# Kernel optimization log

Hardware: AMD Instinct MI355X
Metric: run time of the kernel (lower is better)

The kernel has to match this reference:

```python
import jax, jax.numpy as jnp
import numpy as np

B, T, D, H = 8, 1024, 512, 8
HD = D // H  # per-head hidden = embed_dim // n_head = 64
EPS = 1e-5


def setup_inputs() -> dict:
    key = jax.random.key(0)
    ks = jax.random.split(key, 8)
    x = jax.random.normal(ks[0], (B, T, D), dtype=jnp.float32)
    sc = 1.0 / np.sqrt(D)
    Wq = jax.random.normal(ks[1], (D, H * HD), dtype=jnp.float32) * sc
    Wk = jax.random.normal(ks[2], (D, H * HD), dtype=jnp.float32) * sc
    Wp = jax.random.normal(ks[3], (H * HD, D), dtype=jnp.float32) * sc
    bq = jnp.zeros((H * HD,), jnp.float32)
    bk = jnp.zeros((H * HD,), jnp.float32)
    bp = jnp.zeros((D,), jnp.float32)
    w_mlp = jax.random.normal(ks[4], (2 * HD,), dtype=jnp.float32) * 0.1
    ln_g = jnp.ones((D,), jnp.float32)
    ln_b = jnp.zeros((D,), jnp.float32)
    return {"x": x, "Wq": Wq, "bq": bq, "Wk": Wk, "bk": bk,
            "Wp": Wp, "bp": bp, "w_mlp": w_mlp, "ln_g": ln_g, "ln_b": ln_b}


def reference(x, Wq, bq, Wk, bk, Wp, bp, w_mlp, ln_g, ln_b):
    b, t, d = x.shape
    h, hd = H, HD
    # q/k projections, split into heads: [B,T,H,hd]
    qx = (x @ Wq + bq).reshape(b, t, h, hd)
    kx = (x @ Wk + bk).reshape(b, t, h, hd)
    # MLP score: tanh(concat(k_j, q_i) . w) == tanh(k_j.w[:hd] + q_i.w[hd:])
    k_s = jnp.einsum('bkhd,d->bkh', kx, w_mlp[:hd])   # [B,K,H]
    q_s = jnp.einsum('bqhd,d->bqh', qx, w_mlp[hd:])   # [B,Q,H]
    score = jnp.tanh(q_s[:, :, None, :] + k_s[:, None, :, :])  # [B,Q,K,H]
    attn = jax.nn.softmax(score, axis=2)  # softmax over k_len
    # values are the key projection kx (bmm(score, kx) in original)
    out = jnp.einsum('bqkh,bkhd->bqhd', attn, kx).reshape(b, t, h * hd)
    out = out @ Wp + bp  # output projection (dropout is identity at eval)
    # residual + LayerNorm
    y = x + out
    mu = jnp.mean(y, axis=-1, keepdims=True)
    var = jnp.var(y, axis=-1, keepdims=True)
    yn = (y - mu) * jax.lax.rsqrt(var + EPS)
    return yn * ln_g + ln_b
```

## Files before the change

### kernel.cpp

```cpp
#include <hip/hip_runtime.h>
#include <cstddef>

#define TT 1024
#define DDIM 512
#define HH 8
#define NND 128
#define NS 68

typedef __attribute__((ext_vector_type(8))) short bfrag;
typedef __attribute__((ext_vector_type(4))) float facc;

#define SC2   2.8853900817779268f
#define L2E   1.4426950408889634f

static __device__ __forceinline__ unsigned bfrne(float f) {
    unsigned u = __float_as_uint(f);
    return (u + 0x7fffu + ((u >> 16) & 1u)) >> 16;
}
static __device__ __forceinline__ unsigned pack2rne(float a, float b) {
    return bfrne(a) | (bfrne(b) << 16);
}
static __device__ __forceinline__ unsigned pack2hu(float a, float b) {
    return ((__float_as_uint(a) + 0x8000u) >> 16) |
           ((__float_as_uint(b) + 0x8000u) & 0xffff0000u);
}
static __device__ __forceinline__ void gl2lds16(const void* g, void* l) {
    __builtin_amdgcn_global_load_lds(
        (const __attribute__((address_space(1))) unsigned int*)g,
        (__attribute__((address_space(3))) unsigned int*)l, 16, 0, 0);
}
static __device__ __forceinline__ float wfun(float z2) {
    float t = __builtin_amdgcn_exp2f(z2);
    float r = __builtin_amdgcn_rcpf(t + 1.f);
    return __builtin_amdgcn_exp2f(fmaf(r, -2.f * L2E, L2E));
}

__global__ __launch_bounds__(256) void prepare_kernel(
    const float* __restrict__ x, const float* __restrict__ Wk,
    const float* __restrict__ Wp, const float* __restrict__ Wq,
    const float* __restrict__ bq, const float* __restrict__ wm,
    unsigned short* __restrict__ xb, unsigned short* __restrict__ WkT,
    unsigned short* __restrict__ WpT, unsigned short* __restrict__ vq2b,
    float* __restrict__ qsb2)
{
    const int bx = blockIdx.x, tid = threadIdx.x;
    if (bx < 2048) {
        const int lane = tid & 63, wave = tid >> 6;
        const int row = bx * 4 + wave;
        const float4* xr = (const float4*)(x + (size_t)row * DDIM);
        float4 x0 = xr[lane * 2], x1 = xr[lane * 2 + 1];
        uint4 st;
        st.x = pack2rne(x0.x, x0.y); st.y = pack2rne(x0.z, x0.w);
        st.z = pack2rne(x1.x, x1.y); st.w = pack2rne(x1.z, x1.w);
        int p = lane ^ (row & 7);
        *(uint4*)(xb + (size_t)row * DDIM + p * 8) = st;
    } else if (bx < 2176) {
        int idx = bx - 2048;
        const float* src = (idx & 64) ? Wp : Wk;
        unsigned short* dst = (idx & 64) ? WpT : WkT;
        idx &= 63;
        const int n0 = (idx & 7) * 64, k0 = (idx >> 3) * 64;
        __shared__ float sT[64][65];
        #pragma unroll
        for (int it = 0; it < 4; ++it) {
            int task = it * 256 + tid;
            int kr = task >> 4, c4 = (task & 15) * 4;
            float4 v = *(const float4*)(src + (size_t)(k0 + kr) * DDIM + n0 + c4);
            sT[kr][c4] = v.x; sT[kr][c4 + 1] = v.y; sT[kr][c4 + 2] = v.z; sT[kr][c4 + 3] = v.w;
        }
        __syncthreads();
        #pragma unroll
        for (int it = 0; it < 2; ++it) {
            int task = it * 256 + tid;
            int n = task >> 3, kg = task & 7;
            unsigned u[4];
            #pragma unroll
            for (int jj = 0; jj < 4; ++jj)
                u[jj] = pack2rne(sT[kg * 8 + jj * 2][n], sT[kg * 8 + jj * 2 + 1][n]);
            int p = ((k0 >> 3) + kg) ^ (n & 7);
            uint4 st; st.x = u[0]; st.y = u[1]; st.z = u[2]; st.w = u[3];
            *(uint4*)(dst + (size_t)(n0 + n) * DDIM + p * 8) = st;
        }
    } else {
        int idx = (bx - 2176) * 256 + tid;
        int h = idx >> 9, d = idx & 511;
        float s = 0.f;
        #pragma unroll 8
        for (int j = 0; j < 64; ++j)
            s = fmaf(Wq[(size_t)d * DDIM + h * 64 + j], wm[64 + j], s);
        vq2b[h * DDIM + d] = (unsigned short)bfrne(s * SC2);
        if (idx < HH) {
            float sb = 0.f;
            for (int j = 0; j < 64; ++j)
                sb = fmaf(bq[idx * 64 + j], wm[64 + j], sb);
            qsb2[idx] = sb * SC2;
        }
    }
}

__global__ __launch_bounds__(256) void gemm1_kernel(
    const unsigned short* __restrict__ A, const unsigned short* __restrict__ B,
    const float* __restrict__ bias, unsigned short* __restrict__ kxTg,
    float* __restrict__ ks2, const float* __restrict__ wm,
    const unsigned short* __restrict__ vq2b, const float* __restrict__ qsb2,
    float* __restrict__ qs2)
{
    __shared__ __align__(16) unsigned short smem[12288];
    unsigned short* sA = smem;
    unsigned short* sB = smem + 8192;
    const int tid = threadIdx.x, lane = tid & 63, wave = tid >> 6;
    const int l15 = lane & 15, quad = lane >> 4;
    const int h = blockIdx.x, row0 = blockIdx.y * 128;
    const int col0 = h * 64;

    facc acc[2][4]; facc accq[2];
    #pragma unroll
    for (int i = 0; i < 2; ++i) {
        #pragma unroll
        for (int j = 0; j < 4; ++j) { acc[i][j][0]=0.f; acc[i][j][1]=0.f; acc[i][j][2]=0.f; acc[i][j][3]=0.f; }
        accq[i][0]=0.f; accq[i][1]=0.f; accq[i][2]=0.f; accq[i][3]=0.f;
    }

    for (int k0 = 0; k0 < 512; k0 += 64) {
        #pragma unroll
        for (int it = 0; it < 4; ++it) {
            int g = it * 256 + tid;
            int r = g >> 3, kg = g & 7;
            gl2lds16(A + (size_t)(row0 + r) * 512 + k0 + kg * 8, &sA[g * 8]);
        }
        #pragma unroll
        for (int it = 0; it < 2; ++it) {
            int g = it * 256 + tid;
            int r = g >> 3, kg = g & 7;
            gl2lds16(B + (size_t)(col0 + r) * 512 + k0 + kg * 8, &sB[g * 8]);
        }
        __syncthreads();
        #pragma unroll
        for (int ks_ = 0; ks_ < 2; ++ks_) {
            int slot = (ks_ * 4 + quad) ^ (l15 & 7);
            bfrag a[2], b[4];
            #pragma unroll
            for (int i = 0; i < 2; ++i)
                a[i] = *(const bfrag*)&sA[(wave * 32 + i * 16 + l15) * 64 + slot * 8];
            #pragma unroll
            for (int nt = 0; nt < 4; ++nt)
                b[nt] = *(const bfrag*)&sB[(nt * 16 + l15) * 64 + slot * 8];
            bfrag bvq = *(const bfrag*)(vq2b + h * 512 + k0 + ks_ * 32 + quad * 8);
            #pragma unroll
            for (int i = 0; i < 2; ++i) {
                #pragma unroll
                for (int nt = 0; nt < 4; ++nt)
                    acc[i][nt] = __builtin_amdgcn_mfma_f32_16x16x32_bf16(a[i], b[nt], acc[i][nt], 0, 0, 0);
                accq[i] = __builtin_amdgcn_mfma_f32_16x16x32_bf16(a[i], bvq, accq[i], 0, 0, 0);
            }
        }
        __syncthreads();
    }

    const int bb = row0 >> 10, t0 = row0 & 1023;
    const float qsbh = qsb2[h];
    float bvv[4], wmv[4];
    #pragma unroll
    for (int nt = 0; nt < 4; ++nt) {
        bvv[nt] = bias[col0 + nt * 16 + l15];
        wmv[nt] = wm[nt * 16 + l15] * SC2;
    }
    float part[2][4];
    #pragma unroll
    for (int i = 0; i < 2; ++i)
        #pragma unroll
        for (int r = 0; r < 4; ++r) part[i][r] = 0.f;

    unsigned short* eT = smem;
    #pragma unroll
    for (int i = 0; i < 2; ++i) {
        int tr = wave * 32 + i * 16 + quad * 4;
        #pragma unroll
        for (int nt = 0; nt < 4; ++nt) {
            int col = nt * 16 + l15;
            float v0 = acc[i][nt][0] + bvv[nt], v1 = acc[i][nt][1] + bvv[nt];
            float v2 = acc[i][nt][2] + bvv[nt], v3 = acc[i][nt][3] + bvv[nt];
            part[i][0] = fmaf(wmv[nt], v0, part[i][0]);
            part[i][1] = fmaf(wmv[nt], v1, part[i][1]);
            part[i][2] = fmaf(wmv[nt], v2, part[i][2]);
            part[i][3] = fmaf(wmv[nt], v3, part[i][3]);
            *(unsigned*)&eT[col * 136 + tr]     = pack2rne(v0, v1);
            *(unsigned*)&eT[col * 136 + tr + 2] = pack2rne(v2, v3);
        }
    }
    #pragma unroll
    for (int i = 0; i < 2; ++i)
        #pragma unroll
        for (int r = 0; r < 4; ++r) {
            float p = part[i][r];
            p += __shfl_xor(p, 1); p += __shfl_xor(p, 2);
            p += __shfl_xor(p, 4); p += __shfl_xor(p, 8);
            if (l15 == 0) {
                size_t o = (size_t)(bb * HH + h) * TT + t0 + wave * 32 + i * 16 + quad * 4 + r;
                ks2[o] = p;
                qs2[o] = accq[i][r] + qsbh;
            }
        }
    __syncthreads();
    unsigned short* kxbase = kxTg + ((size_t)(bb * HH + h) * 64) * TT;
    #pragma unroll
    for (int it = 0; it < 4; ++it) {
        int task = it * 256 + tid;
        int col = task >> 4, seg = task & 15;
        uint4 v = *(const uint4*)&eT[col * 136 + seg * 8];
        int g = (t0 >> 3) + seg;
        int p = g ^ (col & 7);
        *(uint4*)(kxbase + (size_t)col * TT + p * 8) = v;
    }
}

__global__ __launch_bounds__(256) void attn_kernel(
    const unsigned short* __restrict__ kxTg, const float* __restrict__ qs2,
    const float* __restrict__ ks2, unsigned short* __restrict__ attb)
{
    __shared__ __align__(16) unsigned short kxT[64 * 256];
    __shared__ float ksc[1024];
    __shared__ float redl[8];
    __shared__ __align__(16) float nodes[NND * NS];
    const int bh = blockIdx.x >> 1, thalf = blockIdx.x & 1;
    const int b = bh >> 3, h = bh & 7;
    const int tid = threadIdx.x, lane = tid & 63, wave = tid >> 6;
    const int l15 = lane & 15, quad = lane >> 4;

    ((float4*)ksc)[tid] = ((const float4*)(ks2 + (size_t)bh * TT))[tid];
    float4 q4 = ((const float4*)(qs2 + (size_t)bh * TT))[tid];
    float mn = fminf(fminf(q4.x, q4.y), fminf(q4.z, q4.w));
    float mx = fmaxf(fmaxf(q4.x, q4.y), fmaxf(q4.z, q4.w));
    #pragma unroll
    for (int off = 32; off > 0; off >>= 1) {
        mn = fminf(mn, __shfl_xor(mn, off));
        mx = fmaxf(mx, __shfl_xor(mx, off));
    }
    if (lane == 0) { redl[wave] = mn; redl[4 + wave] = mx; }
    __syncthreads();
    const float mnv = fminf(fminf(redl[0], redl[1]), fminf(redl[2], redl[3]));
    const float mxv = fmaxf(fmaxf(redl[4], redl[5]), fmaxf(redl[6], redl[7]));
    const float h2v = (mxv - mnv) * (1.f / 127.f);
    const float inv127v = 127.f / fmaxf(mxv - mnv, 1e-12f);
    const float zA = mnv + (wave * 16 + l15) * h2v;
    const float zB = zA + 64.f * h2v;

    const unsigned short* kxbase = kxTg + (size_t)bh * 64 * TT;
    facc acc[2][4]; facc accZ[2];
    #pragma unroll
    for (int g = 0; g < 2; ++g) {
        #pragma unroll
        for (int i = 0; i < 4; ++i) { acc[g][i][0]=0.f; acc[g][i][1]=0.f; acc[g][i][2]=0.f; acc[g][i][3]=0.f; }
        accZ[g][0]=0.f; accZ[g][1]=0.f; accZ[g][2]=0.f; accZ[g][3]=0.f;
    }
    bfrag ones;
    #pragma unroll
    for (int j = 0; j < 8; ++j) ones[j] = (short)0x3F80;

    for (int ck = 0; ck < 4; ++ck) {
        #pragma unroll
        for (int it = 0; it < 8; ++it) {
            int g = it * 256 + tid;
            int d = g >> 5, j = g & 31;
            gl2lds16(kxbase + (size_t)d * TT + ck * 256 + j * 8, &kxT[g * 8]);
        }
        __syncthreads();
        #pragma unroll
        for (int kst = 0; kst < 8; ++kst) {
            const float* kvp = &ksc[ck * 256 + kst * 32 + quad * 8];
            float4 kv0 = *(const float4*)kvp;
            float4 kv1 = *(const float4*)(kvp + 4);
            int slot = (kst * 4 + quad) ^ (l15 & 7);
            bfrag bf_[4];
            #pragma unroll
            for (int dt = 0; dt < 4; ++dt)
                bf_[dt] = *(const bfrag*)&kxT[(dt * 16 + l15) * 256 + slot * 8];
            #pragma unroll
            for (int g = 0; g < 2; ++g) {
                float z = g ? zB : zA;
                union { unsigned u[4]; bfrag f; } afu;
                afu.u[0] = pack2hu(wfun(z + kv0.x), wfun(z + kv0.y));
                afu.u[1] = pack2hu(wfun(z + kv0.z), wfun(z + kv0.w));
                afu.u[2] = pack2hu(wfun(z + kv1.x), wfun(z + kv1.y));
                afu.u[3] = pack2hu(wfun(z + kv1.z), wfun(z + kv1.w));
                #pragma unroll
                for (int dt = 0; dt < 4; ++dt)
                    acc[g][dt] = __builtin_amdgcn_mfma_f32_16x16x32_bf16(afu.f, bf_[dt], acc[g][dt], 0, 0, 0);
                accZ[g] = __builtin_amdgcn_mfma_f32_16x16x32_bf16(afu.f, ones, accZ[g], 0, 0, 0);
            }
        }
        __syncthreads();
    }
    #pragma unroll
    for (int g = 0; g < 2; ++g) {
        #pragma unroll
        for (int r = 0; r < 4; ++r) {
            int node = g * 64 + wave * 16 + quad * 4 + r;
            #pragma unroll
            for (int dt = 0; dt < 4; ++dt)
                nodes[node * NS + dt * 16 + l15] = acc[g][dt][r];
            if (l15 == 0) nodes[node * NS + 64] = accZ[g][r];
        }
    }
    __syncthreads();

    const float* qsp = qs2 + (size_t)bh * TT;
    #pragma unroll 2
    for (int it = 0; it < 32; ++it) {
        int task = it * 256 + tid;
        int t = thalf * 512 + (task >> 4), dp = task & 15;
        float qv = qsp[t];
        float u = (qv - mnv) * inv127v;
        int i = (int)floorf(u) - 1;
        i = i < 0 ? 0 : (i > NND - 4 ? NND - 4 : i);
        float s = u - (float)i;
        float s1 = s - 1.f, s2 = s - 2.f, s3 = s - 3.f;
        float w0 = -s1 * s2 * s3 * (1.f / 6.f);
        float w1 = s * s2 * s3 * 0.5f;
        float w2 = -s * s1 * s3 * 0.5f;
        float w3 = s * s1 * s2 * (1.f / 6.f);
        const float* base = &nodes[i * NS];
        float4 v0 = *(const float4*)(base + 4 * dp);
        float4 v1 = *(const float4*)(base + NS + 4 * dp);
        float4 v2 = *(const float4*)(base + 2 * NS + 4 * dp);
        float4 v3 = *(const float4*)(base + 3 * NS + 4 * dp);
        float zz = w0 * base[64] + w1 * base[NS + 64] + w2 * base[2 * NS + 64] + w3 * base[3 * NS + 64];
        float ox = w0 * v0.x + w1 * v1.x + w2 * v2.x + w3 * v3.x;
        float oy = w0 * v0.y + w1 * v1.y + w2 * v2.y + w3 * v3.y;
        float oz = w0 * v0.z + w1 * v1.z + w2 * v2.z + w3 * v3.z;
        float ow = w0 * v0.w + w1 * v1.w + w2 * v2.w + w3 * v3.w;
        float rz = __builtin_amdgcn_rcpf(zz);
        uint2 st;
        st.x = pack2rne(ox * rz, oy * rz);
        st.y = pack2rne(oz * rz, ow * rz);
        int row = b * TT + t;
        int col = h * 64 + 4 * dp;
        int p = (col >> 3) ^ (row & 7);
        *(uint2*)&attb[(size_t)row * DDIM + p * 8 + (col & 7)] = st;
    }
}

__global__ __launch_bounds__(256) void gemm2_kernel(
    const unsigned short* __restrict__ A, const unsigned short* __restrict__ B,
    const float* __restrict__ bias, const float* __restrict__ x,
    unsigned short* __restrict__ yb)
{
    __shared__ __align__(16) unsigned short smem[12288];
    unsigned short* sA = smem;
    unsigned short* sB = smem + 8192;
    const int tid = threadIdx.x, lane = tid & 63, wave = tid >> 6;
    const int l15 = lane & 15, quad = lane >> 4;
    const int col0 = blockIdx.x * 64, row0 = blockIdx.y * 128;

    facc acc[2][4];
    #pragma unroll
    for (int i = 0; i < 2; ++i)
        #pragma unroll
        for (int j = 0; j < 4; ++j) { acc[i][j][0]=0.f; acc[i][j][1]=0.f; acc[i][j][2]=0.f; acc[i][j][3]=0.f; }

    for (int k0 = 0; k0 < 512; k0 += 64) {
        #pragma unroll
        for (int it = 0; it < 4; ++it) {
            int g = it * 256 + tid;
            int r = g >> 3, kg = g & 7;
            gl2lds16(A + (size_t)(row0 + r) * 512 + k0 + kg * 8, &sA[g * 8]);
        }
        #pragma unroll
        for (int it = 0; it < 2; ++it) {
            int g = it * 256 + tid;
            int r = g >> 3, kg = g & 7;
            gl2lds16(B + (size_t)(col0 + r) * 512 + k0 + kg * 8, &sB[g * 8]);
        }
        __syncthreads();
        #pragma unroll
        for (int ks_ = 0; ks_ < 2; ++ks_) {
            int slot = (ks_ * 4 + quad) ^ (l15 & 7);
            bfrag a[2], b[4];
            #pragma unroll
            for (int i = 0; i < 2; ++i)
                a[i] = *(const bfrag*)&sA[(wave * 32 + i * 16 + l15) * 64 + slot * 8];
            #pragma unroll
            for (int nt = 0; nt < 4; ++nt)
                b[nt] = *(const bfrag*)&sB[(nt * 16 + l15) * 64 + slot * 8];
            #pragma unroll
            for (int i = 0; i < 2; ++i)
                #pragma unroll
                for (int nt = 0; nt < 4; ++nt)
                    acc[i][nt] = __builtin_amdgcn_mfma_f32_16x16x32_bf16(a[i], b[nt], acc[i][nt], 0, 0, 0);
        }
        __syncthreads();
    }
    float bvv[4];
    #pragma unroll
    for (int nt = 0; nt < 4; ++nt) bvv[nt] = bias[col0 + nt * 16 + l15];
    unsigned short* yT = smem;
    #pragma unroll
    for (int i = 0; i < 2; ++i) {
        #pragma unroll
        for (int nt = 0; nt < 4; ++nt) {
            int col = nt * 16 + l15;
            #pragma unroll
            for (int r = 0; r < 4; ++r) {
                int row = wave * 32 + i * 16 + quad * 4 + r;
                float xv = x[(size_t)(row0 + row) * DDIM + col0 + col];
                float y = acc[i][nt][r] + bvv[nt] + xv;
                yT[row * 72 + col] = (unsigned short)bfrne(y);
            }
        }
    }
    __syncthreads();
    #pragma unroll
    for (int it = 0; it < 4; ++it) {
        int task = it * 256 + tid;
        int row = task >> 3, seg = task & 7;
        uint4 v = *(const uint4*)&yT[row * 72 + seg * 8];
        *(uint4*)(yb + (size_t)(row0 + row) * DDIM + col0 + seg * 8) = v;
    }
}

__global__ __launch_bounds__(256) void ln_kernel(
    const unsigned short* __restrict__ yb, const float* __restrict__ g,
    const float* __restrict__ bet, float* __restrict__ out)
{
    const int tid = threadIdx.x, lane = tid & 63, wave = tid >> 6;
    const int row = blockIdx.x * 4 + wave;
    uint4 v = *(const uint4*)(yb + (size_t)row * DDIM + lane * 8);
    float y[8];
    y[0] = __uint_as_float(v.x << 16); y[1] = __uint_as_float(v.x & 0xffff0000u);
    y[2] = __uint_as_float(v.y << 16); y[3] = __uint_as_float(v.y & 0xffff0000u);
    y[4] = __uint_as_float(v.z << 16); y[5] = __uint_as_float(v.z & 0xffff0000u);
    y[6] = __uint_as_float(v.w << 16); y[7] = __uint_as_float(v.w & 0xffff0000u);
    float s = 0.f, s2 = 0.f;
    #pragma unroll
    for (int i = 0; i < 8; ++i) { s += y[i]; s2 = fmaf(y[i], y[i], s2); }
    #pragma unroll
    for (int off = 32; off > 0; off >>= 1) {
        s += __shfl_xor(s, off);
        s2 += __shfl_xor(s2, off);
    }
    float mu = s * (1.f / 512.f);
    float var = s2 * (1.f / 512.f) - mu * mu;
    float inv = rsqrtf(var + 1e-5f);
    const float4* gp = (const float4*)(g + lane * 8);
    const float4* bp = (const float4*)(bet + lane * 8);
    float4 g0 = gp[0], g1 = gp[1], b0 = bp[0], b1 = bp[1];
    float4 o0, o1;
    o0.x = (y[0] - mu) * inv * g0.x + b0.x; o0.y = (y[1] - mu) * inv * g0.y + b0.y;
    o0.z = (y[2] - mu) * inv * g0.z + b0.z; o0.w = (y[3] - mu) * inv * g0.w + b0.w;
    o1.x = (y[4] - mu) * inv * g1.x + b1.x; o1.y = (y[5] - mu) * inv * g1.y + b1.y;
    o1.z = (y[6] - mu) * inv * g1.z + b1.z; o1.w = (y[7] - mu) * inv * g1.w + b1.w;
    float4* op = (float4*)(out + (size_t)row * DDIM);
    op[lane * 2] = o0; op[lane * 2 + 1] = o1;
}

extern "C" void kernel_launch(void* const* d_in, const int* in_sizes, int n_in,
                              void* d_out, int out_size, void* d_ws, size_t ws_size,
                              hipStream_t stream)
{
    const float* x    = (const float*)d_in[0];
    const float* Wq   = (const float*)d_in[1];
    const float* bq   = (const float*)d_in[2];
    const float* Wk   = (const float*)d_in[3];
    const float* bk   = (const float*)d_in[4];
    const float* Wp   = (const float*)d_in[5];
    const float* bp   = (const float*)d_in[6];
    const float* wm   = (const float*)d_in[7];
    const float* ln_g = (const float*)d_in[8];
    const float* ln_b = (const float*)d_in[9];
    float* out = (float*)d_out;

    float* ws = (float*)d_ws;
    float*          qsb2 = ws;
    unsigned short* vq2b = (unsigned short*)(ws + 64);
    unsigned short* WkT  = (unsigned short*)(ws + 2112);
    unsigned short* WpT  = (unsigned short*)(ws + 133184);
    unsigned short* xb   = (unsigned short*)(ws + 264256);
    unsigned short* kxTg = (unsigned short*)(ws + 2361408);
    float*          qs2  = ws + 4458560;
    float*          ks2  = ws + 4524096;
    unsigned short* attb = (unsigned short*)(ws + 4589632);
    unsigned short* yb   = xb;

    prepare_kernel<<<2192, 256, 0, stream>>>(x, Wk, Wp, Wq, bq, wm,
                                             xb, WkT, WpT, vq2b, qsb2);
    gemm1_kernel<<<dim3(8, 64), 256, 0, stream>>>(xb, WkT, bk, kxTg, ks2, wm,
                                                  vq2b, qsb2, qs2);
    attn_kernel<<<128, 256, 0, stream>>>(kxTg, qs2, ks2, attb);
    gemm2_kernel<<<dim3(8, 64), 256, 0, stream>>>(attb, WpT, bp, x, yb);
    ln_kernel<<<2048, 256, 0, stream>>>(yb, ln_g, ln_b, out);
}
```

Measured before the change: 153.1 us.

## Widen GEMM tiles to 128x128 and move residual add into LayerNorm

Both projection GEMMs now use 128x128 output tiles computed by a 2x2 wave grid, replacing 128x64 tiles. Each block covers two heads in gemm1 and twice the columns in gemm2, which raises operand reuse per LDS load but halves the block count to 256. The residual add moves out of the gemm2 epilogue into the LayerNorm kernel, which reads the already-swizzled bf16 copy of x rather than fp32 x. This trades residual precision for less traffic, and needs a separate yb buffer. The attention grid is also remapped to a 2D launch.

```diff
diff --git a/kernel.cpp b/kernel.cpp
--- a/kernel.cpp
+++ b/kernel.cpp
@@ -105,17 +105,18 @@
     const unsigned short* __restrict__ vq2b, const float* __restrict__ qsb2,
     float* __restrict__ qs2)
 {
-    __shared__ __align__(16) unsigned short smem[12288];
+    __shared__ __align__(16) unsigned short smem[17408];
     unsigned short* sA = smem;
     unsigned short* sB = smem + 8192;
     const int tid = threadIdx.x, lane = tid & 63, wave = tid >> 6;
     const int l15 = lane & 15, quad = lane >> 4;
-    const int h = blockIdx.x, row0 = blockIdx.y * 128;
-    const int col0 = h * 64;
-
-    facc acc[2][4]; facc accq[2];
-    #pragma unroll
-    for (int i = 0; i < 2; ++i) {
+    const int wr = wave >> 1, wc = wave & 1;
+    const int row0 = blockIdx.x * 128, colpair = blockIdx.y;
+    const int h = colpair * 2 + wc, n0 = colpair * 128;
+
+    facc acc[4][4]; facc accq[4];
+    #pragma unroll
+    for (int i = 0; i < 4; ++i) {
         #pragma unroll
         for (int j = 0; j < 4; ++j) { acc[i][j][0]=0.f; acc[i][j][1]=0.f; acc[i][j][2]=0.f; acc[i][j][3]=0.f; }
         accq[i][0]=0.f; accq[i][1]=0.f; accq[i][2]=0.f; accq[i][3]=0.f;
@@ -127,27 +128,21 @@
             int g = it * 256 + tid;
             int r = g >> 3, kg = g & 7;
             gl2lds16(A + (size_t)(row0 + r) * 512 + k0 + kg * 8, &sA[g * 8]);
-        }
-        #pragma unroll
-        for (int it = 0; it < 2; ++it) {
-            int g = it * 256 + tid;
-            int r = g >> 3, kg = g & 7;
-            gl2lds16(B + (size_t)(col0 + r) * 512 + k0 + kg * 8, &sB[g * 8]);
+            gl2lds16(B + (size_t)(n0 + r) * 512 + k0 + kg * 8, &sB[g * 8]);
         }
         __syncthreads();
         #pragma unroll
         for (int ks_ = 0; ks_ < 2; ++ks_) {
             int slot = (ks_ * 4 + quad) ^ (l15 & 7);
-            bfrag a[2], b[4];
-            #pragma unroll
-            for (int i = 0; i < 2; ++i)
-                a[i] = *(const bfrag*)&sA[(wave * 32 + i * 16 + l15) * 64 + slot * 8];
-            #pragma unroll
-            for (int nt = 0; nt < 4; ++nt)
-                b[nt] = *(const bfrag*)&sB[(nt * 16 + l15) * 64 + slot * 8];
+            bfrag a[4], b[4];
+            #pragma unroll
+            for (int i = 0; i < 4; ++i) {
+                a[i] = *(const bfrag*)&sA[(wr * 64 + i * 16 + l15) * 64 + slot * 8];
+                b[i] = *(const bfrag*)&sB[(wc * 64 + i * 16 + l15) * 64 + slot * 8];
+            }
             bfrag bvq = *(const bfrag*)(vq2b + h * 512 + k0 + ks_ * 32 + quad * 8);
             #pragma unroll
-            for (int i = 0; i < 2; ++i) {
+            for (int i = 0; i < 4; ++i) {
                 #pragma unroll
                 for (int nt = 0; nt < 4; ++nt)
                     acc[i][nt] = __builtin_amdgcn_mfma_f32_16x16x32_bf16(a[i], b[nt], acc[i][nt], 0, 0, 0);
@@ -162,55 +157,56 @@
     float bvv[4], wmv[4];
     #pragma unroll
     for (int nt = 0; nt < 4; ++nt) {
-        bvv[nt] = bias[col0 + nt * 16 + l15];
+        bvv[nt] = bias[h * 64 + nt * 16 + l15];
         wmv[nt] = wm[nt * 16 + l15] * SC2;
     }
-    float part[2][4];
-    #pragma unroll
-    for (int i = 0; i < 2; ++i)
+    float part[4][4];
+    #pragma unroll
+    for (int i = 0; i < 4; ++i)
         #pragma unroll
         for (int r = 0; r < 4; ++r) part[i][r] = 0.f;
 
-    unsigned short* eT = smem;
-    #pragma unroll
-    for (int i = 0; i < 2; ++i) {
-        int tr = wave * 32 + i * 16 + quad * 4;
+    unsigned short* eT = smem + wc * 8704;
+    #pragma unroll
+    for (int i = 0; i < 4; ++i) {
+        int tr = wr * 64 + i * 16 + quad * 4;
         #pragma unroll
         for (int nt = 0; nt < 4; ++nt) {
-            int col = nt * 16 + l15;
+            int d = nt * 16 + l15;
             float v0 = acc[i][nt][0] + bvv[nt], v1 = acc[i][nt][1] + bvv[nt];
             float v2 = acc[i][nt][2] + bvv[nt], v3 = acc[i][nt][3] + bvv[nt];
             part[i][0] = fmaf(wmv[nt], v0, part[i][0]);
             part[i][1] = fmaf(wmv[nt], v1, part[i][1]);
             part[i][2] = fmaf(wmv[nt], v2, part[i][2]);
             part[i][3] = fmaf(wmv[nt], v3, part[i][3]);
-            *(unsigned*)&eT[col * 136 + tr]     = pack2rne(v0, v1);
-            *(unsigned*)&eT[col * 136 + tr + 2] = pack2rne(v2, v3);
-        }
-    }
-    #pragma unroll
-    for (int i = 0; i < 2; ++i)
+            *(unsigned*)&eT[d * 136 + tr]     = pack2rne(v0, v1);
+            *(unsigned*)&eT[d * 136 + tr + 2] = pack2rne(v2, v3);
+        }
+    }
+    #pragma unroll
+    for (int i = 0; i < 4; ++i)
         #pragma unroll
         for (int r = 0; r < 4; ++r) {
             float p = part[i][r];
             p += __shfl_xor(p, 1); p += __shfl_xor(p, 2);
             p += __shfl_xor(p, 4); p += __shfl_xor(p, 8);
             if (l15 == 0) {
-                size_t o = (size_t)(bb * HH + h) * TT + t0 + wave * 32 + i * 16 + quad * 4 + r;
+                size_t o = (size_t)(bb * HH + h) * TT + t0 + wr * 64 + i * 16 + quad * 4 + r;
                 ks2[o] = p;
                 qs2[o] = accq[i][r] + qsbh;
             }
         }
     __syncthreads();
-    unsigned short* kxbase = kxTg + ((size_t)(bb * HH + h) * 64) * TT;
-    #pragma unroll
-    for (int it = 0; it < 4; ++it) {
+    #pragma unroll
+    for (int it = 0; it < 8; ++it) {
         int task = it * 256 + tid;
-        int col = task >> 4, seg = task & 15;
-        uint4 v = *(const uint4*)&eT[col * 136 + seg * 8];
+        int hh = task >> 10, rem = task & 1023;
+        int col = rem >> 4, seg = rem & 15;
+        uint4 v = *(const uint4*)&smem[hh * 8704 + col * 136 + seg * 8];
+        int hg = colpair * 2 + hh;
         int g = (t0 >> 3) + seg;
         int p = g ^ (col & 7);
-        *(uint4*)(kxbase + (size_t)col * TT + p * 8) = v;
+        *(uint4*)(kxTg + ((size_t)(bb * HH + hg) * 64 + col) * TT + p * 8) = v;
     }
 }
 
@@ -222,7 +218,7 @@
     __shared__ float ksc[1024];
     __shared__ float redl[8];
     __shared__ __align__(16) float nodes[NND * NS];
-    const int bh = blockIdx.x >> 1, thalf = blockIdx.x & 1;
+    const int bh = blockIdx.x, thalf = blockIdx.y;
     const int b = bh >> 3, h = bh & 7;
     const int tid = threadIdx.x, lane = tid & 63, wave = tid >> 6;
     const int l15 = lane & 15, quad = lane >> 4;
@@ -342,19 +338,19 @@
 
 __global__ __launch_bounds__(256) void gemm2_kernel(
     const unsigned short* __restrict__ A, const unsigned short* __restrict__ B,
-    const float* __restrict__ bias, const float* __restrict__ x,
-    unsigned short* __restrict__ yb)
-{
-    __shared__ __align__(16) unsigned short smem[12288];
+    const float* __restrict__ bias, unsigned short* __restrict__ yb)
+{
+    __shared__ __align__(16) unsigned short smem[17408];
     unsigned short* sA = smem;
     unsigned short* sB = smem + 8192;
     const int tid = threadIdx.x, lane = tid & 63, wave = tid >> 6;
     const int l15 = lane & 15, quad = lane >> 4;
-    const int col0 = blockIdx.x * 64, row0 = blockIdx.y * 128;
-
-    facc acc[2][4];
-    #pragma unroll
-    for (int i = 0; i < 2; ++i)
+    const int wr = wave >> 1, wc = wave & 1;
+    const int row0 = blockIdx.x * 128, col0 = blockIdx.y * 128;
+
+    facc acc[4][4];
+    #pragma unroll
+    for (int i = 0; i < 4; ++i)
         #pragma unroll
         for (int j = 0; j < 4; ++j) { acc[i][j][0]=0.f; acc[i][j][1]=0.f; acc[i][j][2]=0.f; acc[i][j][3]=0.f; }
 
@@ -364,26 +360,20 @@
             int g = it * 256 + tid;
             int r = g >> 3, kg = g & 7;
             gl2lds16(A + (size_t)(row0 + r) * 512 + k0 + kg * 8, &sA[g * 8]);
-        }
-        #pragma unroll
-        for (int it = 0; it < 2; ++it) {
-            int g = it * 256 + tid;
-            int r = g >> 3, kg = g & 7;
             gl2lds16(B + (size_t)(col0 + r) * 512 + k0 + kg * 8, &sB[g * 8]);
         }
         __syncthreads();
         #pragma unroll
         for (int ks_ = 0; ks_ < 2; ++ks_) {
             int slot = (ks_ * 4 + quad) ^ (l15 & 7);
-            bfrag a[2], b[4];
-            #pragma unroll
-            for (int i = 0; i < 2; ++i)
-                a[i] = *(const bfrag*)&sA[(wave * 32 + i * 16 + l15) * 64 + slot * 8];
-            #pragma unroll
-            for (int nt = 0; nt < 4; ++nt)
-                b[nt] = *(const bfrag*)&sB[(nt * 16 + l15) * 64 + slot * 8];
-            #pragma unroll
-            for (int i = 0; i < 2; ++i)
+            bfrag a[4], b[4];
+            #pragma unroll
+            for (int i = 0; i < 4; ++i) {
+                a[i] = *(const bfrag*)&sA[(wr * 64 + i * 16 + l15) * 64 + slot * 8];
+                b[i] = *(const bfrag*)&sB[(wc * 64 + i * 16 + l15) * 64 + slot * 8];
+            }
+            #pragma unroll
+            for (int i = 0; i < 4; ++i)
                 #pragma unroll
                 for (int nt = 0; nt < 4; ++nt)
                     acc[i][nt] = __builtin_amdgcn_mfma_f32_16x16x32_bf16(a[i], b[nt], acc[i][nt], 0, 0, 0);
@@ -392,44 +382,48 @@
     }
     float bvv[4];
     #pragma unroll
-    for (int nt = 0; nt < 4; ++nt) bvv[nt] = bias[col0 + nt * 16 + l15];
+    for (int nt = 0; nt < 4; ++nt) bvv[nt] = bias[col0 + wc * 64 + nt * 16 + l15];
     unsigned short* yT = smem;
     #pragma unroll
-    for (int i = 0; i < 2; ++i) {
+    for (int i = 0; i < 4; ++i) {
         #pragma unroll
         for (int nt = 0; nt < 4; ++nt) {
-            int col = nt * 16 + l15;
+            int col = wc * 64 + nt * 16 + l15;
             #pragma unroll
             for (int r = 0; r < 4; ++r) {
-                int row = wave * 32 + i * 16 + quad * 4 + r;
-                float xv = x[(size_t)(row0 + row) * DDIM + col0 + col];
-                float y = acc[i][nt][r] + bvv[nt] + xv;
-                yT[row * 72 + col] = (unsigned short)bfrne(y);
+                int row = wr * 64 + i * 16 + quad * 4 + r;
+                yT[row * 136 + col] = (unsigned short)bfrne(acc[i][nt][r] + bvv[nt]);
             }
         }
     }
     __syncthreads();
     #pragma unroll
-    for (int it = 0; it < 4; ++it) {
+    for (int it = 0; it < 8; ++it) {
         int task = it * 256 + tid;
-        int row = task >> 3, seg = task & 7;
-        uint4 v = *(const uint4*)&yT[row * 72 + seg * 8];
+        int row = task >> 4, seg = task & 15;
+        uint4 v = *(const uint4*)&yT[row * 136 + seg * 8];
         *(uint4*)(yb + (size_t)(row0 + row) * DDIM + col0 + seg * 8) = v;
     }
 }
 
 __global__ __launch_bounds__(256) void ln_kernel(
-    const unsigned short* __restrict__ yb, const float* __restrict__ g,
-    const float* __restrict__ bet, float* __restrict__ out)
+    const unsigned short* __restrict__ yb, const unsigned short* __restrict__ xb,
+    const float* __restrict__ g, const float* __restrict__ bet,
+    float* __restrict__ out)
 {
     const int tid = threadIdx.x, lane = tid & 63, wave = tid >> 6;
     const int row = blockIdx.x * 4 + wave;
-    uint4 v = *(const uint4*)(yb + (size_t)row * DDIM + lane * 8);
+    uint4 pv = *(const uint4*)(yb + (size_t)row * DDIM + lane * 8);
+    int pgr = lane ^ (row & 7);
+    uint4 xv = *(const uint4*)(xb + (size_t)row * DDIM + pgr * 8);
     float y[8];
-    y[0] = __uint_as_float(v.x << 16); y[1] = __uint_as_float(v.x & 0xffff0000u);
-    y[2] = __uint_as_float(v.y << 16); y[3] = __uint_as_float(v.y & 0xffff0000u);
-    y[4] = __uint_as_float(v.z << 16); y[5] = __uint_as_float(v.z & 0xffff0000u);
-    y[6] = __uint_as_float(v.w << 16); y[7] = __uint_as_float(v.w & 0xffff0000u);
+    const unsigned* pu = (const unsigned*)&pv;
+    const unsigned* xu = (const unsigned*)&xv;
+    #pragma unroll
+    for (int j = 0; j < 4; ++j) {
+        y[2*j]   = __uint_as_float(pu[j] << 16)        + __uint_as_float(xu[j] << 16);
+        y[2*j+1] = __uint_as_float(pu[j] & 0xffff0000u) + __uint_as_float(xu[j] & 0xffff0000u);
+    }
     float s = 0.f, s2 = 0.f;
     #pragma unroll
     for (int i = 0; i < 8; ++i) { s += y[i]; s2 = fmaf(y[i], y[i], s2); }
@@ -479,13 +473,13 @@
     float*          qs2  = ws + 4458560;
     float*          ks2  = ws + 4524096;
     unsigned short* attb = (unsigned short*)(ws + 4589632);
-    unsigned short* yb   = xb;
+    unsigned short* yb   = (unsigned short*)(ws + 6686784);
 
     prepare_kernel<<<2192, 256, 0, stream>>>(x, Wk, Wp, Wq, bq, wm,
                                              xb, WkT, WpT, vq2b, qsb2);
-    gemm1_kernel<<<dim3(8, 64), 256, 0, stream>>>(xb, WkT, bk, kxTg, ks2, wm,
+    gemm1_kernel<<<dim3(64, 4), 256, 0, stream>>>(xb, WkT, bk, kxTg, ks2, wm,
                                                   vq2b, qsb2, qs2);
-    attn_kernel<<<128, 256, 0, stream>>>(kxTg, qs2, ks2, attb);
-    gemm2_kernel<<<dim3(8, 64), 256, 0, stream>>>(attb, WpT, bp, x, yb);
-    ln_kernel<<<2048, 256, 0, stream>>>(yb, ln_g, ln_b, out);
-}
+    attn_kernel<<<dim3(64, 2), 256, 0, stream>>>(kxTg, qs2, ks2, attb);
+    gemm2_kernel<<<dim3(64, 4), 256, 0, stream>>>(attb, WpT, bp, yb);
+    ln_kernel<<<2048, 256, 0, stream>>>(yb, xb, ln_g, ln_b, out);
+}
```

Measured after the change: 151.1 us. No clear change (-1.3%).
